# Kernel optimization log

Hardware: AMD Instinct MI355X
Metric: run time of the kernel (lower is better)

Reference implementation:

```python
import jax, jax.numpy as jnp
import numpy as np

N_NODES = 50000
EMB = 256
HEADS = 8
NEG_SLOPE = 0.2


def gat_conv(x, src, dst, W, a_src, a_dst, b, num_nodes):
    # x: [N, Din]; W: [Din, H, F]; a_src/a_dst: [H, F]; b: [H*F]
    h = jnp.einsum('nd,dhf->nhf', x, W)                      # [N, H, F]
    al_s = jnp.sum(h * a_src, axis=-1)                       # [N, H]
    al_d = jnp.sum(h * a_dst, axis=-1)                       # [N, H]
    logits = jax.nn.leaky_relu(al_s[src] + al_d[dst], NEG_SLOPE)  # [E, H]
    # segment softmax over incoming edges of each destination node
    m = jax.ops.segment_max(logits, dst, num_segments=num_nodes)  # [N, H]
    e = jnp.exp(logits - m[dst])                              # [E, H]
    z = jax.ops.segment_sum(e, dst, num_segments=num_nodes)   # [N, H]
    alpha = e / (z[dst] + 1e-16)                              # [E, H]
    msg = h[src] * alpha[..., None]                           # [E, H, F]
    out = jax.ops.segment_sum(msg, dst, num_segments=num_nodes)  # [N, H, F]
    return out.reshape(num_nodes, -1) + b


def setup_inputs() -> dict:
    key = jax.random.key(0)
    ks = jax.random.split(key, 10)
    F1 = EMB // HEADS  # 32
    x = jax.random.normal(ks[0], (N_NODES, EMB), dtype=jnp.float32)
    edge_index = jax.random.randint(ks[1], (2, 800000), 0, N_NODES, dtype=jnp.int64)
    s1 = 1.0 / np.sqrt(EMB)
    W1 = jax.random.normal(ks[2], (EMB, HEADS, F1), dtype=jnp.float32) * s1
    a_src1 = jax.random.normal(ks[3], (HEADS, F1), dtype=jnp.float32) * s1
    a_dst1 = jax.random.normal(ks[4], (HEADS, F1), dtype=jnp.float32) * s1
    b1 = jnp.zeros((HEADS * F1,), dtype=jnp.float32)
    W2 = jax.random.normal(ks[5], (EMB, 1, EMB), dtype=jnp.float32) * s1
    a_src2 = jax.random.normal(ks[6], (1, EMB), dtype=jnp.float32) * s1
    a_dst2 = jax.random.normal(ks[7], (1, EMB), dtype=jnp.float32) * s1
    b2 = jnp.zeros((EMB,), dtype=jnp.float32)
    return {"x": x, "edge_index": edge_index,
            "W1": W1, "a_src1": a_src1, "a_dst1": a_dst1, "b1": b1,
            "W2": W2, "a_src2": a_src2, "a_dst2": a_dst2, "b2": b2}


def reference(x, edge_index, W1, a_src1, a_dst1, b1, W2, a_src2, a_dst2, b2):
    n = x.shape[0]
    loops = jnp.arange(n, dtype=edge_index.dtype)
    src = jnp.concatenate([edge_index[0], loops])
    dst = jnp.concatenate([edge_index[1], loops])
    h = gat_conv(x, src, dst, W1, a_src1, a_dst1, b1, n)   # [N, EMB]
    out = gat_conv(h, src, dst, W2, a_src2, a_dst2, b2, n)  # [N, EMB]
    return out
```

## Files before the change

kernel.cpp:

```cpp
#include <hip/hip_runtime.h>
#include <hip/hip_bf16.h>

typedef unsigned short u16;
typedef unsigned int   u32;

typedef __attribute__((ext_vector_type(8))) short s16x8;
typedef __attribute__((ext_vector_type(8))) unsigned short u16x8;
typedef __attribute__((ext_vector_type(4))) float f32x4;

#define CAP 64

__device__ __forceinline__ float b2f(u16 u) {
    union { u32 i; float f; } v; v.i = ((u32)u) << 16; return v.f;
}
__device__ __forceinline__ u16 f2b(float f) {
    union { float f; u32 i; } v; v.f = f;
    u32 u = v.i;
    u32 r = (u + 0x7fffu + ((u >> 16) & 1u)) >> 16;
    return (u16)r;
}

__device__ __forceinline__ int detect_f32(const u16* xw) {
    int t = threadIdx.x & 63;
    u16 w = xw[2 * t];
    int e = (w >> 7) & 0xFF;
    bool sane = (e >= 112 && e <= 131);
    unsigned long long m1 = __ballot(sane);
    return (__popcll(m1) >= 32) ? 0 : 1;
}

__device__ __forceinline__ int edge_at(const int* __restrict__ ei, int i64f, long long j) {
    return i64f ? ei[2 * j] : ei[(size_t)j];
}

__global__ __launch_bounds__(256) void prep(const void* __restrict__ x,
                                            const int* __restrict__ ei,
                                            const void* __restrict__ W1, const void* __restrict__ W2,
                                            const void* p0, const void* p1, const void* p2,
                                            const void* p3, const void* p4, const void* p5,
                                            u16* __restrict__ xb, u16* __restrict__ wt1,
                                            u16* __restrict__ wt2, u16* __restrict__ sv,
                                            int* __restrict__ cur, int* __restrict__ csr,
                                            int* __restrict__ flags,
                                            int x4, int BX, int ZB, int CF, int NN) {
    int b = blockIdx.x, t = threadIdx.x;
    int f32f = detect_f32((const u16*)x);
    if (b < BX) {
        int i = b * 256 + t;
        if (i < x4) {
            ushort4 o;
            if (f32f) {
                float4 v = ((const float4*)x)[i];
                o.x = f2b(v.x); o.y = f2b(v.y); o.z = f2b(v.z); o.w = f2b(v.w);
            } else o = ((const ushort4*)x)[i];
            ((ushort4*)xb)[i] = o;
        }
        return;
    }
    b -= BX;
    if (b < 512) {
        const void* W = (b < 256) ? W1 : W2;
        u16* Wt = (b < 256) ? wt1 : wt2;
        int k = b & 255;
        u16 v = f32f ? f2b(((const float*)W)[k * 256 + t]) : ((const u16*)W)[k * 256 + t];
        Wt[t * 256 + k] = v;
        return;
    }
    b -= 512;
    if (b == 0) {
        const void* ps[6] = {p0, p1, p2, p3, p4, p5};
#pragma unroll
        for (int j = 0; j < 6; j++) {
            u16 v = f32f ? f2b(((const float*)ps[j])[t]) : ((const u16*)ps[j])[t];
            sv[j * 256 + t] = v;
        }
        if (t < 64) {
            bool hz = (ei[2 * t + 1] == 0);
            unsigned long long m2 = __ballot(hz);
            if (t == 0) {
                flags[0] = f32f;
                flags[1] = (m2 == ~0ull) ? 1 : 0;
            }
        }
        return;
    }
    b -= 1;
    if (b < ZB) {
        int i = b * 256 + t;
        if (i < (NN + 3) / 4) ((int4*)cur)[i] = make_int4(0, 0, 0, 0);
        return;
    }
    b -= ZB;
    if (b < CF) {
        int i = b * 256 + t;
        ((int4*)csr)[i] = make_int4(NN, NN, NN, NN);
        return;
    }
}

__global__ __launch_bounds__(256) void fill_csr(const int* __restrict__ ei,
                                                int* __restrict__ cur,
                                                int* __restrict__ csr, int E, int ET,
                                                const int* __restrict__ flags) {
    int i = blockIdx.x * 256 + threadIdx.x;
    if (i >= ET) return;
    int i64f = flags[1];
    int s, d;
    if (i < E) { s = edge_at(ei, i64f, i); d = edge_at(ei, i64f, (long long)E + i); }
    else       { s = d = i - E; }
    int p = atomicAdd(&cur[d], 1);
    if (p < CAP) csr[d * CAP + p] = s;
}

__global__ __launch_bounds__(256) void gemm_tiled(const u16* __restrict__ A,
                                                  const u16* __restrict__ Bt,
                                                  u16* __restrict__ C, int M) {
    __shared__ u16 sA[128 * 32];
    __shared__ u16 sB[128 * 32];
    int tid = threadIdx.x;
    int mt = blockIdx.x >> 1, nt = blockIdx.x & 1;
    int r0 = mt * 128, c0 = nt * 128;
    int w = tid >> 6, lane = tid & 63;
    int wr = w & 1, wc = w >> 1;
    int lm = lane & 15, quad = lane >> 4;

    int row0 = tid >> 2, ch0 = tid & 3;
    int row1 = row0 + 64;
    int ga0 = r0 + row0; if (ga0 >= M) ga0 = M - 1;
    int ga1 = r0 + row1; if (ga1 >= M) ga1 = M - 1;
    const u16* Ab0 = A + (size_t)ga0 * 256 + ch0 * 8;
    const u16* Ab1 = A + (size_t)ga1 * 256 + ch0 * 8;
    const u16* Bb0 = Bt + (size_t)(c0 + row0) * 256 + ch0 * 8;
    const u16* Bb1 = Bt + (size_t)(c0 + row1) * 256 + ch0 * 8;

    u16x8 ra0 = *(const u16x8*)Ab0;
    u16x8 ra1 = *(const u16x8*)Ab1;
    u16x8 rb0 = *(const u16x8*)Bb0;
    u16x8 rb1 = *(const u16x8*)Bb1;

    f32x4 acc[4][4];
#pragma unroll
    for (int i = 0; i < 4; i++)
#pragma unroll
        for (int j = 0; j < 4; j++) acc[i][j] = (f32x4){0.f, 0.f, 0.f, 0.f};

    u16* wA0 = sA + row0 * 32 + ch0 * 8;
    u16* wA1 = sA + row1 * 32 + ch0 * 8;
    u16* wB0 = sB + row0 * 32 + ch0 * 8;
    u16* wB1 = sB + row1 * 32 + ch0 * 8;
    const u16* rA = sA + (wr * 64 + lm) * 32 + quad * 8;
    const u16* rB = sB + (wc * 64 + lm) * 32 + quad * 8;

    for (int kb = 0; kb < 8; kb++) {
        __syncthreads();
        *(u16x8*)wA0 = ra0;
        *(u16x8*)wA1 = ra1;
        *(u16x8*)wB0 = rb0;
        *(u16x8*)wB1 = rb1;
        __syncthreads();
        if (kb < 7) {
            int ko = (kb + 1) * 32;
            ra0 = *(const u16x8*)(Ab0 + ko);
            ra1 = *(const u16x8*)(Ab1 + ko);
            rb0 = *(const u16x8*)(Bb0 + ko);
            rb1 = *(const u16x8*)(Bb1 + ko);
        }
        s16x8 af[4], bf[4];
#pragma unroll
        for (int fr = 0; fr < 4; fr++) af[fr] = *(const s16x8*)(rA + fr * 16 * 32);
#pragma unroll
        for (int fc = 0; fc < 4; fc++) bf[fc] = *(const s16x8*)(rB + fc * 16 * 32);
#pragma unroll
        for (int fr = 0; fr < 4; fr++)
#pragma unroll
            for (int fc = 0; fc < 4; fc++)
                acc[fr][fc] = __builtin_amdgcn_mfma_f32_16x16x32_bf16(af[fr], bf[fc], acc[fr][fc], 0, 0, 0);
    }

#pragma unroll
    for (int fr = 0; fr < 4; fr++) {
#pragma unroll
        for (int fc = 0; fc < 4; fc++) {
#pragma unroll
            for (int r = 0; r < 4; r++) {
                int row = r0 + wr * 64 + fr * 16 + quad * 4 + r;
                if (row < M) C[(size_t)row * 256 + c0 + wc * 64 + fc * 16 + lm] = f2b(acc[fr][fc][r]);
            }
        }
    }
}

__global__ __launch_bounds__(256) void coeff256(const u16* __restrict__ h,
                                                const u16* __restrict__ a_s,
                                                const u16* __restrict__ a_d,
                                                float* __restrict__ al_s,
                                                float* __restrict__ al_d, int N, int H) {
    int tid = threadIdx.x;
    if (blockIdx.x == 0 && tid < 8) al_s[(size_t)N * H + tid] = -1e30f;
    int wid = tid >> 6, lane = tid & 63;
    int node = blockIdx.x * 4 + wid;
    if (node >= N) return;
    ushort4 hv = *(const ushort4*)(h + (size_t)node * 256 + lane * 4);
    ushort4 as = *(const ushort4*)(a_s + lane * 4);
    ushort4 ad = *(const ushort4*)(a_d + lane * 4);
    float h0 = b2f(hv.x), h1 = b2f(hv.y), h2 = b2f(hv.z), h3 = b2f(hv.w);
    float ps = h0 * b2f(as.x) + h1 * b2f(as.y) + h2 * b2f(as.z) + h3 * b2f(as.w);
    float pd = h0 * b2f(ad.x) + h1 * b2f(ad.y) + h2 * b2f(ad.z) + h3 * b2f(ad.w);
    int gsz = 64 / H;
    for (int m = 1; m < gsz; m <<= 1) {
        ps += __shfl_xor(ps, m, 64);
        pd += __shfl_xor(pd, m, 64);
    }
    if ((lane & (gsz - 1)) == 0) {
        int hh = lane / gsz;
        al_s[(size_t)node * H + hh] = ps;
        al_d[(size_t)node * H + hh] = pd;
    }
}

template <int H, int FINAL>
__global__ __launch_bounds__(256) void gat_agg(const u16* __restrict__ hsrc,
                                               const float* __restrict__ al_s,
                                               const float* __restrict__ al_d,
                                               const int* __restrict__ degv,
                                               const int* __restrict__ csr,
                                               const u16* __restrict__ bias,
                                               u16* __restrict__ out_b16,
                                               void* __restrict__ out_final,
                                               const int* __restrict__ flags, int N) {
    int wid = threadIdx.x >> 6, lane = threadIdx.x & 63;
    int c = lane * 4;
    int hc = (H == 8) ? (lane >> 3) : 0;
    int he = lane & (H - 1);
    int j8 = lane >> 3;
    const u16* hb = hsrc + c;
    ushort4 bv = *(const ushort4*)(bias + c);
    int f32f = FINAL ? flags[0] : 0;
    int step = gridDim.x * 4;

    for (int n = blockIdx.x * 4 + wid; n < N; n += step) {
        int deg = degv[n];
        deg = deg < CAP ? deg : CAP;
        int beg = n * CAP;
        int end = beg + ((deg + 7) & ~7);
        float ad_e = al_d[(size_t)n * H + he];
        float a0 = 0.f, a1 = 0.f, a2 = 0.f, a3 = 0.f, z = 0.f;

        int i = beg;
        for (; i + 16 <= end; i += 16) {
            int sma = csr[i + j8];
            int smb = csr[i + 8 + j8];
            float va = al_s[(size_t)sma * H + he] + ad_e;
            float vb = al_s[(size_t)smb * H + he] + ad_e;
            va = va > 0.f ? va : 0.2f * va;
            vb = vb > 0.f ? vb : 0.2f * vb;
            float ea = __expf(va);
            float eb = __expf(vb);
#pragma unroll
            for (int j = 0; j < 8; j++) {
                int   sj = __shfl(sma, j * 8, 64);
                float ej = __shfl(ea, j * 8 + hc, 64);
                ushort4 hv = *(const ushort4*)(hb + (size_t)sj * 256);
                z += ej;
                a0 += ej * b2f(hv.x); a1 += ej * b2f(hv.y);
                a2 += ej * b2f(hv.z); a3 += ej * b2f(hv.w);
            }
#pragma unroll
            for (int j = 0; j < 8; j++) {
                int   sj = __shfl(smb, j * 8, 64);
                float ej = __shfl(eb, j * 8 + hc, 64);
                ushort4 hv = *(const ushort4*)(hb + (size_t)sj * 256);
                z += ej;
                a0 += ej * b2f(hv.x); a1 += ej * b2f(hv.y);
                a2 += ej * b2f(hv.z); a3 += ej * b2f(hv.w);
            }
        }
        if (i < end) {
            int sm = csr[i + j8];
            float v = al_s[(size_t)sm * H + he] + ad_e;
            v = v > 0.f ? v : 0.2f * v;
            float em = __expf(v);
#pragma unroll
            for (int j = 0; j < 8; j++) {
                int   sj = __shfl(sm, j * 8, 64);
                float ej = __shfl(em, j * 8 + hc, 64);
                ushort4 hv = *(const ushort4*)(hb + (size_t)sj * 256);
                z += ej;
                a0 += ej * b2f(hv.x); a1 += ej * b2f(hv.y);
                a2 += ej * b2f(hv.z); a3 += ej * b2f(hv.w);
            }
        }

        float invz = 1.f / (z + 1e-16f);
        float o0 = a0 * invz + b2f(bv.x);
        float o1 = a1 * invz + b2f(bv.y);
        float o2 = a2 * invz + b2f(bv.z);
        float o3 = a3 * invz + b2f(bv.w);
        if (FINAL) {
            if (f32f) {
                float4 ov; ov.x = o0; ov.y = o1; ov.z = o2; ov.w = o3;
                ((float4*)out_final)[(size_t)n * 64 + lane] = ov;
            } else {
                ushort4 ov; ov.x = f2b(o0); ov.y = f2b(o1); ov.z = f2b(o2); ov.w = f2b(o3);
                ((ushort4*)out_final)[(size_t)n * 64 + lane] = ov;
            }
        } else {
            ushort4 ov; ov.x = f2b(o0); ov.y = f2b(o1); ov.z = f2b(o2); ov.w = f2b(o3);
            ((ushort4*)out_b16)[(size_t)n * 64 + lane] = ov;
        }
    }
}

extern "C" void kernel_launch(void* const* d_in, const int* in_sizes, int n_in,
                              void* d_out, int out_size, void* d_ws, size_t ws_size,
                              hipStream_t stream) {
    (void)n_in; (void)out_size; (void)ws_size;
    const void* x   = d_in[0];
    const int*  ei  = (const int*)d_in[1];
    const void* W1  = d_in[2];
    const void* as1 = d_in[3];
    const void* ad1 = d_in[4];
    const void* b1  = d_in[5];
    const void* W2  = d_in[6];
    const void* as2 = d_in[7];
    const void* ad2 = d_in[8];
    const void* b2  = d_in[9];

    const int N  = in_sizes[0] / 256;
    const int E  = in_sizes[1] / 2;
    const int ET = E + N;

    char* base = (char*)d_ws;
    size_t o = 0;
    auto carve = [&](size_t bytes) -> void* {
        void* q = base + o;
        o += (bytes + 255) & ~(size_t)255;
        return q;
    };
    u16*   hproj = (u16*)carve((size_t)(N + 1) * 256 * 2);
    float* als   = (float*)carve((size_t)(N + 1) * 8 * 4);
    float* ald   = (float*)carve((size_t)N * 8 * 4);
    int*   cur   = (int*)carve(((size_t)N + 16) * 4);
    int*   csr   = (int*)carve((size_t)N * CAP * 4);
    u16*   wt1   = (u16*)carve(256 * 256 * 2);
    u16*   wt2   = (u16*)carve(256 * 256 * 2);
    u16*   sv    = (u16*)carve(6 * 256 * 2);
    int*   flags = (int*)carve(16 * 4);

    u16* xb = (u16*)d_out;

    int x4 = N * 256 / 4;
    int BX = (x4 + 255) / 256;
    int ZB = ((N + 3) / 4 + 255) / 256;
    int CF = (N * CAP / 4 + 255) / 256;
    int PB = BX + 512 + 1 + ZB + CF;
    prep<<<PB, 256, 0, stream>>>(x, ei, W1, W2, as1, ad1, b1, as2, ad2, b2,
                                 xb, wt1, wt2, sv, cur, csr, flags,
                                 x4, BX, ZB, CF, N);

    int cg = (ET + 255) / 256;
    fill_csr<<<cg, 256, 0, stream>>>(ei, cur, csr, E, ET, flags);

    int gt = ((N + 127) / 128) * 2;
    int ab = (N + 3) / 4;
    int agb = 2048;
    gemm_tiled<<<gt, 256, 0, stream>>>(xb, wt1, hproj, N);
    coeff256<<<ab, 256, 0, stream>>>(hproj, sv + 0 * 256, sv + 1 * 256, als, ald, N, 8);
    gat_agg<8, 0><<<agb, 256, 0, stream>>>(hproj, als, ald, cur, csr, sv + 2 * 256,
                                           xb, nullptr, flags, N);
    gemm_tiled<<<gt, 256, 0, stream>>>(xb, wt2, hproj, N);
    coeff256<<<ab, 256, 0, stream>>>(hproj, sv + 3 * 256, sv + 4 * 256, als, ald, N, 1);
    gat_agg<1, 1><<<agb, 256, 0, stream>>>(hproj, als, ald, cur, csr, sv + 5 * 256,
                                           nullptr, d_out, flags, N);
}
```

Measured before the change: 370.9 us.

## Store CSR as u16, head-major attention coeffs, per-head column-slice aggregation

```diff
diff --git a/kernel.cpp b/kernel.cpp
--- a/kernel.cpp
+++ b/kernel.cpp
@@ -40,8 +40,8 @@
                                             const void* p3, const void* p4, const void* p5,
                                             u16* __restrict__ xb, u16* __restrict__ wt1,
                                             u16* __restrict__ wt2, u16* __restrict__ sv,
-                                            int* __restrict__ cur, int* __restrict__ csr,
-                                            int* __restrict__ flags,
+                                            int* __restrict__ cur, u16* __restrict__ csr,
+                                            int* __restrict__ flags, u16* __restrict__ hp,
                                             int x4, int BX, int ZB, int CF, int NN) {
     int b = blockIdx.x, t = threadIdx.x;
     int f32f = detect_f32((const u16*)x);
@@ -74,6 +74,7 @@
             u16 v = f32f ? f2b(((const float*)ps[j])[t]) : ((const u16*)ps[j])[t];
             sv[j * 256 + t] = v;
         }
+        hp[(size_t)NN * 256 + t] = 0;
         if (t < 64) {
             bool hz = (ei[2 * t + 1] == 0);
             unsigned long long m2 = __ballot(hz);
@@ -93,14 +94,15 @@
     b -= ZB;
     if (b < CF) {
         int i = b * 256 + t;
-        ((int4*)csr)[i] = make_int4(NN, NN, NN, NN);
+        int pat = (NN & 0xFFFF) | (NN << 16);
+        if (i < NN * (CAP / 8)) ((int4*)csr)[i] = make_int4(pat, pat, pat, pat);
         return;
     }
 }
 
 __global__ __launch_bounds__(256) void fill_csr(const int* __restrict__ ei,
                                                 int* __restrict__ cur,
-                                                int* __restrict__ csr, int E, int ET,
+                                                u16* __restrict__ csr, int E, int ET,
                                                 const int* __restrict__ flags) {
     int i = blockIdx.x * 256 + threadIdx.x;
     if (i >= ET) return;
@@ -109,7 +111,7 @@
     if (i < E) { s = edge_at(ei, i64f, i); d = edge_at(ei, i64f, (long long)E + i); }
     else       { s = d = i - E; }
     int p = atomicAdd(&cur[d], 1);
-    if (p < CAP) csr[d * CAP + p] = s;
+    if (p < CAP) csr[d * CAP + p] = (u16)s;
 }
 
 __global__ __launch_bounds__(256) void gemm_tiled(const u16* __restrict__ A,
@@ -196,7 +198,7 @@
                                                 float* __restrict__ al_s,
                                                 float* __restrict__ al_d, int N, int H) {
     int tid = threadIdx.x;
-    if (blockIdx.x == 0 && tid < 8) al_s[(size_t)N * H + tid] = -1e30f;
+    if (blockIdx.x == 0 && tid < 8) al_s[(size_t)tid * (N + 1) + N] = -1e30f;
     int wid = tid >> 6, lane = tid & 63;
     int node = blockIdx.x * 4 + wid;
     if (node >= N) return;
@@ -213,100 +215,100 @@
     }
     if ((lane & (gsz - 1)) == 0) {
         int hh = lane / gsz;
-        al_s[(size_t)node * H + hh] = ps;
-        al_d[(size_t)node * H + hh] = pd;
+        al_s[(size_t)hh * (N + 1) + node] = ps;
+        al_d[(size_t)hh * N + node] = pd;
     }
 }
 
 template <int H, int FINAL>
 __global__ __launch_bounds__(256) void gat_agg(const u16* __restrict__ hsrc,
-                                               const float* __restrict__ al_s,
-                                               const float* __restrict__ al_d,
+                                               const float* __restrict__ als,
+                                               const float* __restrict__ ald,
                                                const int* __restrict__ degv,
-                                               const int* __restrict__ csr,
+                                               const u16* __restrict__ csr16,
                                                const u16* __restrict__ bias,
                                                u16* __restrict__ out_b16,
                                                void* __restrict__ out_final,
                                                const int* __restrict__ flags, int N) {
-    int wid = threadIdx.x >> 6, lane = threadIdx.x & 63;
-    int c = lane * 4;
-    int hc = (H == 8) ? (lane >> 3) : 0;
-    int he = lane & (H - 1);
-    int j8 = lane >> 3;
-    const u16* hb = hsrc + c;
-    ushort4 bv = *(const ushort4*)(bias + c);
+    int tid = threadIdx.x;
+    int wid = tid >> 6, lane = tid & 63;
+    int k = lane >> 4, sub = lane & 15;
+    int j = sub >> 2, c = sub & 3;
+    int slice = blockIdx.x & 7;
+    int col0 = slice * 32 + c * 8;
+    int hd = (H == 8) ? slice : 0;
+    const float* as_h = als + (size_t)hd * (N + 1);
+    const float* ad_h = ald + (size_t)hd * N;
+    const u16* hb = hsrc + col0;
+    float bf[8];
+    {
+        u16x8 bv = *(const u16x8*)(bias + col0);
+#pragma unroll
+        for (int q = 0; q < 8; q++) bf[q] = b2f(bv[q]);
+    }
     int f32f = FINAL ? flags[0] : 0;
-    int step = gridDim.x * 4;
-
-    for (int n = blockIdx.x * 4 + wid; n < N; n += step) {
+    int step = (gridDim.x >> 3) * 16;
+
+    for (int n = (blockIdx.x >> 3) * 16 + wid * 4 + k; n < N; n += step) {
         int deg = degv[n];
         deg = deg < CAP ? deg : CAP;
         int beg = n * CAP;
-        int end = beg + ((deg + 7) & ~7);
-        float ad_e = al_d[(size_t)n * H + he];
-        float a0 = 0.f, a1 = 0.f, a2 = 0.f, a3 = 0.f, z = 0.f;
+        int end = beg + ((deg + 3) & ~3);
+        float ad_e = ad_h[n];
+        float a[8];
+#pragma unroll
+        for (int q = 0; q < 8; q++) a[q] = 0.f;
+        float z = 0.f;
+
+        auto body = [&](int i) {
+            int sm = csr16[i + j];
+            float v = as_h[sm] + ad_e;
+            v = v > 0.f ? v : 0.2f * v;
+            float e = __expf(v);
+            u16x8 hv = *(const u16x8*)(hb + (size_t)sm * 256);
+            z += e;
+#pragma unroll
+            for (int q = 0; q < 8; q++) a[q] += e * b2f(hv[q]);
+        };
 
         int i = beg;
-        for (; i + 16 <= end; i += 16) {
-            int sma = csr[i + j8];
-            int smb = csr[i + 8 + j8];
-            float va = al_s[(size_t)sma * H + he] + ad_e;
-            float vb = al_s[(size_t)smb * H + he] + ad_e;
-            va = va > 0.f ? va : 0.2f * va;
-            vb = vb > 0.f ? vb : 0.2f * vb;
-            float ea = __expf(va);
-            float eb = __expf(vb);
-#pragma unroll
-            for (int j = 0; j < 8; j++) {
-                int   sj = __shfl(sma, j * 8, 64);
-                float ej = __shfl(ea, j * 8 + hc, 64);
-                ushort4 hv = *(const ushort4*)(hb + (size_t)sj * 256);
-                z += ej;
-                a0 += ej * b2f(hv.x); a1 += ej * b2f(hv.y);
-                a2 += ej * b2f(hv.z); a3 += ej * b2f(hv.w);
+        for (; i + 8 <= end; i += 8) {
+            body(i);
+            body(i + 4);
+        }
+        if (i < end) body(i);
+
+#pragma unroll
+        for (int m = 4; m <= 8; m <<= 1) {
+            z += __shfl_xor(z, m, 64);
+#pragma unroll
+            for (int q = 0; q < 8; q++) a[q] += __shfl_xor(a[q], m, 64);
+        }
+
+        if (j == 0) {
+            float invz = 1.f / (z + 1e-16f);
+            float o[8];
+#pragma unroll
+            for (int q = 0; q < 8; q++) o[q] = a[q] * invz + bf[q];
+            if (FINAL) {
+                if (f32f) {
+                    float4 v0 = make_float4(o[0], o[1], o[2], o[3]);
+                    float4 v1 = make_float4(o[4], o[5], o[6], o[7]);
+                    size_t bi = (size_t)n * 64 + (col0 >> 2);
+                    ((float4*)out_final)[bi]     = v0;
+                    ((float4*)out_final)[bi + 1] = v1;
+                } else {
+                    u16x8 ov;
+#pragma unroll
+                    for (int q = 0; q < 8; q++) ov[q] = f2b(o[q]);
+                    *(u16x8*)((u16*)out_final + (size_t)n * 256 + col0) = ov;
+                }
+            } else {
+                u16x8 ov;
+#pragma unroll
+                for (int q = 0; q < 8; q++) ov[q] = f2b(o[q]);
+                *(u16x8*)(out_b16 + (size_t)n * 256 + col0) = ov;
             }
-#pragma unroll
-            for (int j = 0; j < 8; j++) {
-                int   sj = __shfl(smb, j * 8, 64);
-                float ej = __shfl(eb, j * 8 + hc, 64);
-                ushort4 hv = *(const ushort4*)(hb + (size_t)sj * 256);
-                z += ej;
-                a0 += ej * b2f(hv.x); a1 += ej * b2f(hv.y);
-                a2 += ej * b2f(hv.z); a3 += ej * b2f(hv.w);
-            }
-        }
-        if (i < end) {
-            int sm = csr[i + j8];
-            float v = al_s[(size_t)sm * H + he] + ad_e;
-            v = v > 0.f ? v : 0.2f * v;
-            float em = __expf(v);
-#pragma unroll
-            for (int j = 0; j < 8; j++) {
-                int   sj = __shfl(sm, j * 8, 64);
-                float ej = __shfl(em, j * 8 + hc, 64);
-                ushort4 hv = *(const ushort4*)(hb + (size_t)sj * 256);
-                z += ej;
-                a0 += ej * b2f(hv.x); a1 += ej * b2f(hv.y);
-                a2 += ej * b2f(hv.z); a3 += ej * b2f(hv.w);
-            }
-        }
-
-        float invz = 1.f / (z + 1e-16f);
-        float o0 = a0 * invz + b2f(bv.x);
-        float o1 = a1 * invz + b2f(bv.y);
-        float o2 = a2 * invz + b2f(bv.z);
-        float o3 = a3 * invz + b2f(bv.w);
-        if (FINAL) {
-            if (f32f) {
-                float4 ov; ov.x = o0; ov.y = o1; ov.z = o2; ov.w = o3;
-                ((float4*)out_final)[(size_t)n * 64 + lane] = ov;
-            } else {
-                ushort4 ov; ov.x = f2b(o0); ov.y = f2b(o1); ov.z = f2b(o2); ov.w = f2b(o3);
-                ((ushort4*)out_final)[(size_t)n * 64 + lane] = ov;
-            }
-        } else {
-            ushort4 ov; ov.x = f2b(o0); ov.y = f2b(o1); ov.z = f2b(o2); ov.w = f2b(o3);
-            ((ushort4*)out_b16)[(size_t)n * 64 + lane] = ov;
         }
     }
 }
@@ -338,10 +340,10 @@
         return q;
     };
     u16*   hproj = (u16*)carve((size_t)(N + 1) * 256 * 2);
-    float* als   = (float*)carve((size_t)(N + 1) * 8 * 4);
-    float* ald   = (float*)carve((size_t)N * 8 * 4);
+    float* als   = (float*)carve((size_t)8 * (N + 1) * 4);
+    float* ald   = (float*)carve((size_t)8 * N * 4);
     int*   cur   = (int*)carve(((size_t)N + 16) * 4);
-    int*   csr   = (int*)carve((size_t)N * CAP * 4);
+    u16*   csr   = (u16*)carve((size_t)N * CAP * 2);
     u16*   wt1   = (u16*)carve(256 * 256 * 2);
     u16*   wt2   = (u16*)carve(256 * 256 * 2);
     u16*   sv    = (u16*)carve(6 * 256 * 2);
@@ -352,10 +354,10 @@
     int x4 = N * 256 / 4;
     int BX = (x4 + 255) / 256;
     int ZB = ((N + 3) / 4 + 255) / 256;
-    int CF = (N * CAP / 4 + 255) / 256;
+    int CF = (N * (CAP / 8) + 255) / 256;
     int PB = BX + 512 + 1 + ZB + CF;
     prep<<<PB, 256, 0, stream>>>(x, ei, W1, W2, as1, ad1, b1, as2, ad2, b2,
-                                 xb, wt1, wt2, sv, cur, csr, flags,
+                                 xb, wt1, wt2, sv, cur, csr, flags, hproj,
                                  x4, BX, ZB, CF, N);
 
     int cg = (ET + 255) / 256;
```

Result: slower. 444.6 us (+19.9%).
